# Performance work log

Measured on AMD Instinct MI355X. Metric: run time of the kernel, lower is better.

The kernel has to match this reference:

```python
import jax, jax.numpy as jnp
import numpy as np

B, T, C = 2, 2048, 1024
H = 16
D = C // H          # head_dim = 64
WIN = 256           # local window


def _rope(x):
    # x: [B, H, T, D]; rotate pairs (even, odd) with per-pair frequencies.
    t = x.shape[2]
    d = x.shape[-1] // 2
    theta = 10000.0 ** (-(jnp.arange(d, dtype=x.dtype) / d))          # [d]
    ang = jnp.arange(t, dtype=x.dtype)[:, None] * theta               # [T, d]
    sin, cos = jnp.sin(ang), jnp.cos(ang)                             # [T, d]
    x1, x2 = x[..., ::2], x[..., 1::2]                                # [B,H,T,d]
    out = jnp.stack([x1 * cos - x2 * sin, x1 * sin + x2 * cos], axis=-1)
    return out.reshape(x.shape)


def setup_inputs() -> dict:
    key = jax.random.key(0)
    k1, k2, k3 = jax.random.split(key, 3)
    s = 1.0 / np.sqrt(C)
    return {
        "x": jax.random.normal(k1, (B, T, C), dtype=jnp.float32),
        "w_qkv": jax.random.normal(k2, (3 * C, C), dtype=jnp.float32) * s,
        "w_out": jax.random.normal(k3, (C, C), dtype=jnp.float32) * s,
        "b_out": jnp.zeros((C,), dtype=jnp.float32),
    }


def reference(x, w_qkv, w_out, b_out):
    b, t, c = x.shape
    qkv = x @ w_qkv.T                                   # [B,T,3C]
    qkv = qkv.reshape(b, t, H, 3 * D).transpose(0, 2, 1, 3)  # [B,H,T,3D]
    q, k, v = jnp.split(qkv, 3, axis=-1)                # each [B,H,T,D]
    q, k = _rope(q), _rope(k)
    scores = jnp.einsum("bhqd,bhkd->bhqk", q, k) / jnp.sqrt(jnp.asarray(D, x.dtype))
    i = jnp.arange(t)[:, None]
    j = jnp.arange(t)[None, :]
    mask = (j <= i) & (j >= i - WIN)                    # causal local window
    scores = jnp.where(mask, scores, -jnp.inf)
    attn = jax.nn.softmax(scores, axis=-1)              # [B,H,T,T]
    out = jnp.einsum("bhqk,bhkd->bhqd", attn, v)        # [B,H,T,D]
    out = out.transpose(0, 2, 1, 3).reshape(b, t, c)    # [B,T,C]
    return out @ w_out.T + b_out
```

## Files before the change

kernel.cpp:

```cpp
#include <hip/hip_runtime.h>
#include <math.h>

#define BB 2
#define TT 2048
#define CC 1024
#define HH 16
#define DD 64
#define WINW 256

constexpr int MROWS  = BB * TT;
constexpr int NQKV   = 3 * CC;
constexpr int QKV_LD = 3 * CC;

typedef unsigned short ushort_t;
typedef __attribute__((ext_vector_type(8))) short  bf16x8;
typedef __attribute__((ext_vector_type(4))) float  f32x4;
typedef __attribute__((ext_vector_type(8))) unsigned short u16x8;

__device__ __forceinline__ float bf2f(ushort_t u) {
    return __uint_as_float(((unsigned int)u) << 16);
}
__device__ __forceinline__ ushort_t f2bf(float f) {
    unsigned int u = __float_as_uint(f);
    u += 0x7fffu + ((u >> 16) & 1u);
    return (ushort_t)(u >> 16);
}

__device__ __forceinline__ void async16(void* lds, const void* g) {
    __builtin_amdgcn_global_load_lds(
        (const __attribute__((address_space(1))) unsigned int*)g,
        (__attribute__((address_space(3))) unsigned int*)lds, 16, 0, 0);
}

__global__ __launch_bounds__(256)
void f32_to_bf16(const float* __restrict__ in, ushort_t* __restrict__ out) {
    int i = (blockIdx.x * 256 + threadIdx.x) * 4;
    float4 v = *(const float4*)&in[i];
    ushort4 o;
    o.x = f2bf(v.x); o.y = f2bf(v.y); o.z = f2bf(v.z); o.w = f2bf(v.w);
    *(ushort4*)&out[i] = o;
}

template <bool BIAS, bool OUT_BF16>
__global__ __launch_bounds__(256)
void gemm_nt_mfma(const ushort_t* __restrict__ A, const ushort_t* __restrict__ Bw,
                  const float* __restrict__ bias, void* __restrict__ Cc,
                  int M, int N, int K) {
    __shared__ __align__(16) ushort_t As[128 * 32];
    __shared__ __align__(16) ushort_t Bs[128 * 32];

    const int tid  = threadIdx.x;
    const int lane = tid & 63;
    const int wv   = tid >> 6;
    const int wr   = wv >> 1;
    const int wc   = wv & 1;
    const int bm   = blockIdx.y * 128;
    const int bn   = blockIdx.x * 128;

    const int srow = tid >> 2;
    const int scol = (tid & 3) * 8;

    const ushort_t* Ag = A + (size_t)(bm + srow) * K + scol;
    const ushort_t* Bg = Bw + (size_t)(bn + srow) * K + scol;

    f32x4 acc[4][4];
#pragma unroll
    for (int m = 0; m < 4; ++m)
#pragma unroll
        for (int n = 0; n < 4; ++n)
            acc[m][n] = f32x4{0.f, 0.f, 0.f, 0.f};

    const int fr = lane & 15;
    const int fq = lane >> 4;

    for (int k0 = 0; k0 < K; k0 += 32) {
        async16(&As[tid * 8],        Ag);
        async16(&As[2048 + tid * 8], Ag + (size_t)64 * K);
        async16(&Bs[tid * 8],        Bg);
        async16(&Bs[2048 + tid * 8], Bg + (size_t)64 * K);
        Ag += 32; Bg += 32;
        __syncthreads();

        bf16x8 af[4], bfv[4];
#pragma unroll
        for (int m = 0; m < 4; ++m)
            af[m] = *(const bf16x8*)&As[(wr * 64 + m * 16 + fr) * 32 + fq * 8];
#pragma unroll
        for (int n = 0; n < 4; ++n)
            bfv[n] = *(const bf16x8*)&Bs[(wc * 64 + n * 16 + fr) * 32 + fq * 8];
#pragma unroll
        for (int m = 0; m < 4; ++m)
#pragma unroll
            for (int n = 0; n < 4; ++n)
                acc[m][n] = __builtin_amdgcn_mfma_f32_16x16x32_bf16(
                    af[m], bfv[n], acc[m][n], 0, 0, 0);
        __syncthreads();
    }

#pragma unroll
    for (int m = 0; m < 4; ++m) {
#pragma unroll
        for (int n = 0; n < 4; ++n) {
            const int col = bn + wc * 64 + n * 16 + fr;
            const float bv = BIAS ? bias[col] : 0.0f;
#pragma unroll
            for (int j = 0; j < 4; ++j) {
                const int row = bm + wr * 64 + m * 16 + fq * 4 + j;
                float v = acc[m][n][j] + bv;
                if (OUT_BF16)
                    ((ushort_t*)Cc)[(size_t)row * N + col] = f2bf(v);
                else
                    ((float*)Cc)[(size_t)row * N + col] = v;
            }
        }
    }
}

__global__ __launch_bounds__(256)
void rope_kernel(ushort_t* __restrict__ qkv) {
    int idx = blockIdx.x * 256 + threadIdx.x;
    int i = idx & 31;
    int h = (idx >> 5) & (HH - 1);
    int t = (idx >> 9) & (TT - 1);
    int b = idx >> 20;

    float theta = powf(10000.0f, -(float)i / 32.0f);
    float ang = (float)t * theta;
    float s, c;
    sincosf(ang, &s, &c);

    ushort_t* row = qkv + (size_t)(b * TT + t) * QKV_LD + h * (3 * DD);
    float q1 = bf2f(row[2 * i]), q2 = bf2f(row[2 * i + 1]);
    row[2 * i]     = f2bf(q1 * c - q2 * s);
    row[2 * i + 1] = f2bf(q1 * s + q2 * c);
    float k1 = bf2f(row[DD + 2 * i]), k2 = bf2f(row[DD + 2 * i + 1]);
    row[DD + 2 * i]     = f2bf(k1 * c - k2 * s);
    row[DD + 2 * i + 1] = f2bf(k1 * s + k2 * c);
}

#define MASKNEG (-1e30f)

__global__ __launch_bounds__(256)
void attn_mfma(const ushort_t* __restrict__ qkv, ushort_t* __restrict__ out) {
    __shared__ __align__(16) ushort_t Ks[64 * 72];
    __shared__ __align__(16) ushort_t Vt[64 * 72];
    __shared__ __align__(16) ushort_t Ps[4][16 * 72];

    const int tid  = threadIdx.x;
    const int lane = tid & 63;
    const int wv   = tid >> 6;
    const int fr   = lane & 15;
    const int fq   = lane >> 4;

    const int blk = blockIdx.x;
    const int qt  = blk & 31;
    const int h   = (blk >> 5) & 15;
    const int b   = blk >> 9;
    const int q0  = qt * 64;

    const ushort_t* base = qkv + (size_t)(b * TT) * QKV_LD + h * (3 * DD);

    bf16x8 qf0, qf1;
    {
        const ushort_t* qrow = base + (size_t)(q0 + wv * 16 + fr) * QKV_LD;
        qf0 = *(const bf16x8*)(qrow + fq * 8);
        qf1 = *(const bf16x8*)(qrow + 32 + fq * 8);
    }

    f32x4 oacc[4];
#pragma unroll
    for (int nd = 0; nd < 4; ++nd) oacc[nd] = f32x4{0.f, 0.f, 0.f, 0.f};
    float mj[4], lj[4];
#pragma unroll
    for (int j = 0; j < 4; ++j) { mj[j] = MASKNEG; lj[j] = 0.f; }

    const int sr = tid >> 2;
    const int sc = (tid & 3) * 16;

    const int kstart = (q0 >= WINW) ? (q0 - WINW) : 0;

    for (int kt0 = kstart; kt0 < q0 + 64; kt0 += 64) {
        __syncthreads();
        {
            const ushort_t* krow = base + (size_t)(kt0 + sr) * QKV_LD + DD + sc;
            u16x8 a = *(const u16x8*)krow;
            u16x8 bvv = *(const u16x8*)(krow + 8);
            *(u16x8*)&Ks[sr * 72 + sc]     = a;
            *(u16x8*)&Ks[sr * 72 + sc + 8] = bvv;
        }
        {
            const ushort_t* vrow = base + (size_t)(kt0 + sr) * QKV_LD + 2 * DD + sc;
            u16x8 a = *(const u16x8*)vrow;
            u16x8 bvv = *(const u16x8*)(vrow + 8);
#pragma unroll
            for (int e = 0; e < 8; ++e) {
                Vt[(sc + e) * 72 + sr]     = a[e];
                Vt[(sc + 8 + e) * 72 + sr] = bvv[e];
            }
        }
        __syncthreads();

        f32x4 s[4];
#pragma unroll
        for (int n = 0; n < 4; ++n) {
            bf16x8 kb0 = *(const bf16x8*)&Ks[(n * 16 + fr) * 72 + fq * 8];
            bf16x8 kb1 = *(const bf16x8*)&Ks[(n * 16 + fr) * 72 + 32 + fq * 8];
            f32x4 z = f32x4{0.f, 0.f, 0.f, 0.f};
            z = __builtin_amdgcn_mfma_f32_16x16x32_bf16(qf0, kb0, z, 0, 0, 0);
            s[n] = __builtin_amdgcn_mfma_f32_16x16x32_bf16(qf1, kb1, z, 0, 0, 0);
        }

        float pmax[4];
#pragma unroll
        for (int j = 0; j < 4; ++j) pmax[j] = MASKNEG;
#pragma unroll
        for (int n = 0; n < 4; ++n) {
            const int key = kt0 + n * 16 + fr;
#pragma unroll
            for (int j = 0; j < 4; ++j) {
                const int qi = q0 + wv * 16 + fq * 4 + j;
                const bool ok = (key <= qi) && (key >= qi - WINW);
                float sv = ok ? s[n][j] * 0.125f : MASKNEG;
                s[n][j] = sv;
                pmax[j] = fmaxf(pmax[j], sv);
            }
        }
#pragma unroll
        for (int off = 1; off < 16; off <<= 1)
#pragma unroll
            for (int j = 0; j < 4; ++j)
                pmax[j] = fmaxf(pmax[j], __shfl_xor(pmax[j], off));

        float tl[4] = {0.f, 0.f, 0.f, 0.f};
#pragma unroll
        for (int j = 0; j < 4; ++j) {
            float mnew = fmaxf(mj[j], pmax[j]);
            float alpha = (mnew <= -1e29f) ? 1.0f : __expf(mj[j] - mnew);
            mj[j] = mnew;
            lj[j] *= alpha;
#pragma unroll
            for (int nd = 0; nd < 4; ++nd) oacc[nd][j] *= alpha;
        }
#pragma unroll
        for (int n = 0; n < 4; ++n) {
#pragma unroll
            for (int j = 0; j < 4; ++j) {
                float sv = s[n][j];
                float p = (sv <= -1e29f) ? 0.f : __expf(sv - mj[j]);
                tl[j] += p;
                Ps[wv][(fq * 4 + j) * 72 + n * 16 + fr] = f2bf(p);
            }
        }
#pragma unroll
        for (int off = 1; off < 16; off <<= 1)
#pragma unroll
            for (int j = 0; j < 4; ++j)
                tl[j] += __shfl_xor(tl[j], off);
#pragma unroll
        for (int j = 0; j < 4; ++j) lj[j] += tl[j];

        bf16x8 pa0 = *(const bf16x8*)&Ps[wv][fr * 72 + fq * 8];
        bf16x8 pa1 = *(const bf16x8*)&Ps[wv][fr * 72 + 32 + fq * 8];
#pragma unroll
        for (int nd = 0; nd < 4; ++nd) {
            bf16x8 vb0 = *(const bf16x8*)&Vt[(nd * 16 + fr) * 72 + fq * 8];
            bf16x8 vb1 = *(const bf16x8*)&Vt[(nd * 16 + fr) * 72 + 32 + fq * 8];
            oacc[nd] = __builtin_amdgcn_mfma_f32_16x16x32_bf16(pa0, vb0, oacc[nd], 0, 0, 0);
            oacc[nd] = __builtin_amdgcn_mfma_f32_16x16x32_bf16(pa1, vb1, oacc[nd], 0, 0, 0);
        }
    }

#pragma unroll
    for (int nd = 0; nd < 4; ++nd) {
#pragma unroll
        for (int j = 0; j < 4; ++j) {
            const int qi = q0 + wv * 16 + fq * 4 + j;
            out[(size_t)(b * TT + qi) * CC + h * DD + nd * 16 + fr] =
                f2bf(oacc[nd][j] / lj[j]);
        }
    }
}

extern "C" void kernel_launch(void* const* d_in, const int* in_sizes, int n_in,
                              void* d_out, int out_size, void* d_ws, size_t ws_size,
                              hipStream_t stream) {
    const float* x     = (const float*)d_in[0];
    const float* w_qkv = (const float*)d_in[1];
    const float* w_out = (const float*)d_in[2];
    const float* b_out = (const float*)d_in[3];
    float* out = (float*)d_out;

    ushort_t* qkv_b  = (ushort_t*)d_ws;
    ushort_t* attn_b = qkv_b  + (size_t)MROWS * NQKV;
    ushort_t* xb     = attn_b + (size_t)MROWS * CC;
    ushort_t* wqb    = xb     + (size_t)MROWS * CC;
    ushort_t* wob    = wqb    + (size_t)NQKV * CC;

    f32_to_bf16<<<(MROWS * CC) / 1024, 256, 0, stream>>>(x, xb);
    f32_to_bf16<<<(NQKV * CC) / 1024, 256, 0, stream>>>(w_qkv, wqb);
    f32_to_bf16<<<(CC * CC) / 1024, 256, 0, stream>>>(w_out, wob);

    gemm_nt_mfma<false, true><<<dim3(NQKV / 128, MROWS / 128), 256, 0, stream>>>(
        xb, wqb, nullptr, qkv_b, MROWS, NQKV, CC);

    rope_kernel<<<(BB * TT * HH * 32) / 256, 256, 0, stream>>>(qkv_b);

    attn_mfma<<<BB * HH * (TT / 64), 256, 0, stream>>>(qkv_b, attn_b);

    gemm_nt_mfma<true, false><<<dim3(CC / 128, MROWS / 128), 256, 0, stream>>>(
        attn_b, wob, b_out, out, MROWS, CC, CC);
}
```

Before: 122.3 us.

## Fuse conversions and RoPE into GEMM epilogue; widen attention tiles with async loads

Merges the three fp32-to-bf16 conversion launches into one kernel and moves RoPE into the QKV GEMM epilogue, using a lane shuffle to fetch the paired element. This removes a separate read-modify-write pass over Q and K. The attention kernel now handles 128 queries with 8 waves per block so each K/V tile is shared by more queries, and it loads K/V straight into LDS with a swizzled layout, transposing V from the staged copy. The cost is an extra barrier per tile and a sincos per output element in the GEMM epilogue.

```diff
diff --git a/kernel.cpp b/kernel.cpp
--- a/kernel.cpp
+++ b/kernel.cpp
@@ -32,16 +32,27 @@
         (__attribute__((address_space(3))) unsigned int*)lds, 16, 0, 0);
 }
 
+constexpr int NX = MROWS * CC;
+constexpr int NQ = NQKV * CC;
+constexpr int NO = CC * CC;
+
 __global__ __launch_bounds__(256)
-void f32_to_bf16(const float* __restrict__ in, ushort_t* __restrict__ out) {
+void convert_all(const float* __restrict__ x, const float* __restrict__ wq,
+                 const float* __restrict__ wo, ushort_t* __restrict__ xb,
+                 ushort_t* __restrict__ wqb, ushort_t* __restrict__ wob) {
     int i = (blockIdx.x * 256 + threadIdx.x) * 4;
-    float4 v = *(const float4*)&in[i];
+    const float* src;
+    ushort_t* dst;
+    if (i < NX)           { src = x  + i;            dst = xb  + i; }
+    else if (i < NX + NQ) { src = wq + (i - NX);     dst = wqb + (i - NX); }
+    else                  { src = wo + (i - NX - NQ); dst = wob + (i - NX - NQ); }
+    float4 v = *(const float4*)src;
     ushort4 o;
     o.x = f2bf(v.x); o.y = f2bf(v.y); o.z = f2bf(v.z); o.w = f2bf(v.w);
-    *(ushort4*)&out[i] = o;
-}
-
-template <bool BIAS, bool OUT_BF16>
+    *(ushort4*)dst = o;
+}
+
+template <bool BIAS, bool OUT_BF16, bool ROPE>
 __global__ __launch_bounds__(256)
 void gemm_nt_mfma(const ushort_t* __restrict__ A, const ushort_t* __restrict__ Bw,
                   const float* __restrict__ bias, void* __restrict__ Cc,
@@ -103,66 +114,69 @@
         for (int n = 0; n < 4; ++n) {
             const int col = bn + wc * 64 + n * 16 + fr;
             const float bv = BIAS ? bias[col] : 0.0f;
+            float vj[4];
+#pragma unroll
+            for (int j = 0; j < 4; ++j) vj[j] = acc[m][n][j] + bv;
+
+            if (ROPE) {
+                float pj[4];
+#pragma unroll
+                for (int j = 0; j < 4; ++j) pj[j] = __shfl_xor(vj[j], 1);
+                const int c = col % 192;
+                if (c < 128) {
+                    const int pi = (c & 63) >> 1;
+                    const float theta = __expf(-0.28782313662425575f * (float)pi);
+                    const bool even = (col & 1) == 0;
+#pragma unroll
+                    for (int j = 0; j < 4; ++j) {
+                        const int row = bm + wr * 64 + m * 16 + fq * 4 + j;
+                        const float t = (float)(row & (TT - 1));
+                        float s, cs;
+                        sincosf(t * theta, &s, &cs);
+                        vj[j] = even ? (vj[j] * cs - pj[j] * s)
+                                     : (pj[j] * s + vj[j] * cs);
+                    }
+                }
+            }
+
 #pragma unroll
             for (int j = 0; j < 4; ++j) {
                 const int row = bm + wr * 64 + m * 16 + fq * 4 + j;
-                float v = acc[m][n][j] + bv;
                 if (OUT_BF16)
-                    ((ushort_t*)Cc)[(size_t)row * N + col] = f2bf(v);
+                    ((ushort_t*)Cc)[(size_t)row * N + col] = f2bf(vj[j]);
                 else
-                    ((float*)Cc)[(size_t)row * N + col] = v;
+                    ((float*)Cc)[(size_t)row * N + col] = vj[j];
             }
         }
     }
 }
 
-__global__ __launch_bounds__(256)
-void rope_kernel(ushort_t* __restrict__ qkv) {
-    int idx = blockIdx.x * 256 + threadIdx.x;
-    int i = idx & 31;
-    int h = (idx >> 5) & (HH - 1);
-    int t = (idx >> 9) & (TT - 1);
-    int b = idx >> 20;
-
-    float theta = powf(10000.0f, -(float)i / 32.0f);
-    float ang = (float)t * theta;
-    float s, c;
-    sincosf(ang, &s, &c);
-
-    ushort_t* row = qkv + (size_t)(b * TT + t) * QKV_LD + h * (3 * DD);
-    float q1 = bf2f(row[2 * i]), q2 = bf2f(row[2 * i + 1]);
-    row[2 * i]     = f2bf(q1 * c - q2 * s);
-    row[2 * i + 1] = f2bf(q1 * s + q2 * c);
-    float k1 = bf2f(row[DD + 2 * i]), k2 = bf2f(row[DD + 2 * i + 1]);
-    row[DD + 2 * i]     = f2bf(k1 * c - k2 * s);
-    row[DD + 2 * i + 1] = f2bf(k1 * s + k2 * c);
-}
-
 #define MASKNEG (-1e30f)
 
-__global__ __launch_bounds__(256)
+__global__ __launch_bounds__(512)
 void attn_mfma(const ushort_t* __restrict__ qkv, ushort_t* __restrict__ out) {
-    __shared__ __align__(16) ushort_t Ks[64 * 72];
+    __shared__ __align__(16) ushort_t Ks[64 * 64];
+    __shared__ __align__(16) ushort_t Vlin[64 * 64];
     __shared__ __align__(16) ushort_t Vt[64 * 72];
-    __shared__ __align__(16) ushort_t Ps[4][16 * 72];
+    __shared__ __align__(16) ushort_t Ps[8][16 * 72];
 
     const int tid  = threadIdx.x;
     const int lane = tid & 63;
-    const int wv   = tid >> 6;
+    const int w    = tid >> 6;
     const int fr   = lane & 15;
     const int fq   = lane >> 4;
 
     const int blk = blockIdx.x;
-    const int qt  = blk & 31;
-    const int h   = (blk >> 5) & 15;
-    const int b   = blk >> 9;
-    const int q0  = qt * 64;
+    const int qt  = blk & 15;
+    const int h   = (blk >> 4) & 15;
+    const int b   = blk >> 8;
+    const int q0  = qt * 128;
 
     const ushort_t* base = qkv + (size_t)(b * TT) * QKV_LD + h * (3 * DD);
 
     bf16x8 qf0, qf1;
     {
-        const ushort_t* qrow = base + (size_t)(q0 + wv * 16 + fr) * QKV_LD;
+        const ushort_t* qrow = base + (size_t)(q0 + w * 16 + fr) * QKV_LD;
         qf0 = *(const bf16x8*)(qrow + fq * 8);
         qf1 = *(const bf16x8*)(qrow + 32 + fq * 8);
     }
@@ -174,37 +188,30 @@
 #pragma unroll
     for (int j = 0; j < 4; ++j) { mj[j] = MASKNEG; lj[j] = 0.f; }
 
-    const int sr = tid >> 2;
-    const int sc = (tid & 3) * 16;
+    const int srow = tid >> 3;
+    const int scol = ((tid & 7) ^ (srow & 7)) * 8;
 
     const int kstart = (q0 >= WINW) ? (q0 - WINW) : 0;
 
-    for (int kt0 = kstart; kt0 < q0 + 64; kt0 += 64) {
-        __syncthreads();
+    for (int kt0 = kstart; kt0 < q0 + 128; kt0 += 64) {
+        __syncthreads();
+        async16(&Ks[tid * 8],   base + (size_t)(kt0 + srow) * QKV_LD + DD + scol);
+        async16(&Vlin[tid * 8], base + (size_t)(kt0 + srow) * QKV_LD + 2 * DD + scol);
+        __syncthreads();
+
         {
-            const ushort_t* krow = base + (size_t)(kt0 + sr) * QKV_LD + DD + sc;
-            u16x8 a = *(const u16x8*)krow;
-            u16x8 bvv = *(const u16x8*)(krow + 8);
-            *(u16x8*)&Ks[sr * 72 + sc]     = a;
-            *(u16x8*)&Ks[sr * 72 + sc + 8] = bvv;
-        }
-        {
-            const ushort_t* vrow = base + (size_t)(kt0 + sr) * QKV_LD + 2 * DD + sc;
-            u16x8 a = *(const u16x8*)vrow;
-            u16x8 bvv = *(const u16x8*)(vrow + 8);
-#pragma unroll
-            for (int e = 0; e < 8; ++e) {
-                Vt[(sc + e) * 72 + sr]     = a[e];
-                Vt[(sc + 8 + e) * 72 + sr] = bvv[e];
-            }
-        }
-        __syncthreads();
+            u16x8 vv = *(const u16x8*)&Vlin[lane * 64 + ((w ^ (lane & 7)) * 8)];
+#pragma unroll
+            for (int e = 0; e < 8; ++e)
+                Vt[(w * 8 + e) * 72 + lane] = vv[e];
+        }
 
         f32x4 s[4];
 #pragma unroll
         for (int n = 0; n < 4; ++n) {
-            bf16x8 kb0 = *(const bf16x8*)&Ks[(n * 16 + fr) * 72 + fq * 8];
-            bf16x8 kb1 = *(const bf16x8*)&Ks[(n * 16 + fr) * 72 + 32 + fq * 8];
+            const int krow = n * 16 + fr;
+            bf16x8 kb0 = *(const bf16x8*)&Ks[krow * 64 + ((fq ^ (krow & 7)) * 8)];
+            bf16x8 kb1 = *(const bf16x8*)&Ks[krow * 64 + (((fq + 4) ^ (krow & 7)) * 8)];
             f32x4 z = f32x4{0.f, 0.f, 0.f, 0.f};
             z = __builtin_amdgcn_mfma_f32_16x16x32_bf16(qf0, kb0, z, 0, 0, 0);
             s[n] = __builtin_amdgcn_mfma_f32_16x16x32_bf16(qf1, kb1, z, 0, 0, 0);
@@ -218,7 +225,7 @@
             const int key = kt0 + n * 16 + fr;
 #pragma unroll
             for (int j = 0; j < 4; ++j) {
-                const int qi = q0 + wv * 16 + fq * 4 + j;
+                const int qi = q0 + w * 16 + fq * 4 + j;
                 const bool ok = (key <= qi) && (key >= qi - WINW);
                 float sv = ok ? s[n][j] * 0.125f : MASKNEG;
                 s[n][j] = sv;
@@ -248,7 +255,7 @@
                 float sv = s[n][j];
                 float p = (sv <= -1e29f) ? 0.f : __expf(sv - mj[j]);
                 tl[j] += p;
-                Ps[wv][(fq * 4 + j) * 72 + n * 16 + fr] = f2bf(p);
+                Ps[w][(fq * 4 + j) * 72 + n * 16 + fr] = f2bf(p);
             }
         }
 #pragma unroll
@@ -259,8 +266,10 @@
 #pragma unroll
         for (int j = 0; j < 4; ++j) lj[j] += tl[j];
 
-        bf16x8 pa0 = *(const bf16x8*)&Ps[wv][fr * 72 + fq * 8];
-        bf16x8 pa1 = *(const bf16x8*)&Ps[wv][fr * 72 + 32 + fq * 8];
+        __syncthreads();
+
+        bf16x8 pa0 = *(const bf16x8*)&Ps[w][fr * 72 + fq * 8];
+        bf16x8 pa1 = *(const bf16x8*)&Ps[w][fr * 72 + 32 + fq * 8];
 #pragma unroll
         for (int nd = 0; nd < 4; ++nd) {
             bf16x8 vb0 = *(const bf16x8*)&Vt[(nd * 16 + fr) * 72 + fq * 8];
@@ -274,7 +283,7 @@
     for (int nd = 0; nd < 4; ++nd) {
 #pragma unroll
         for (int j = 0; j < 4; ++j) {
-            const int qi = q0 + wv * 16 + fq * 4 + j;
+            const int qi = q0 + w * 16 + fq * 4 + j;
             out[(size_t)(b * TT + qi) * CC + h * DD + nd * 16 + fr] =
                 f2bf(oacc[nd][j] / lj[j]);
         }
@@ -296,17 +305,14 @@
     ushort_t* wqb    = xb     + (size_t)MROWS * CC;
     ushort_t* wob    = wqb    + (size_t)NQKV * CC;
 
-    f32_to_bf16<<<(MROWS * CC) / 1024, 256, 0, stream>>>(x, xb);
-    f32_to_bf16<<<(NQKV * CC) / 1024, 256, 0, stream>>>(w_qkv, wqb);
-    f32_to_bf16<<<(CC * CC) / 1024, 256, 0, stream>>>(w_out, wob);
-
-    gemm_nt_mfma<false, true><<<dim3(NQKV / 128, MROWS / 128), 256, 0, stream>>>(
+    convert_all<<<(NX + NQ + NO) / 1024, 256, 0, stream>>>(
+        x, w_qkv, w_out, xb, wqb, wob);
+
+    gemm_nt_mfma<false, true, true><<<dim3(NQKV / 128, MROWS / 128), 256, 0, stream>>>(
         xb, wqb, nullptr, qkv_b, MROWS, NQKV, CC);
 
-    rope_kernel<<<(BB * TT * HH * 32) / 256, 256, 0, stream>>>(qkv_b);
-
-    attn_mfma<<<BB * HH * (TT / 64), 256, 0, stream>>>(qkv_b, attn_b);
-
-    gemm_nt_mfma<true, false><<<dim3(CC / 128, MROWS / 128), 256, 0, stream>>>(
+    attn_mfma<<<BB * HH * (TT / 128), 512, 0, stream>>>(qkv_b, attn_b);
+
+    gemm_nt_mfma<true, false, false><<<dim3(CC / 128, MROWS / 128), 256, 0, stream>>>(
         attn_b, wob, b_out, out, MROWS, CC, CC);
 }
```

New measurement: 145.6 us. 19.1% more time.
